# Kernel tuning notes

Hardware: AMD Instinct MI355X
Metric: run time of the kernel (lower is better)

## Reference

```python
import jax, jax.numpy as jnp
import numpy as np

H1, W1GRID, K_SIZE, B = 28, 28, 5, 512
K2 = K_SIZE * K_SIZE  # 25 kernel weight matrices
_BITS = np.array([[0, 0], [0, 1], [1, 0], [1, 1]])  # 2^dim basis combos


def _grid_edges(h, w):
    """8-neighborhood grid graph; returns (src, dst, pseudo in [0,1]^2)."""
    ys, xs = np.meshgrid(np.arange(h), np.arange(w), indexing='ij')
    node = (ys * w + xs).reshape(-1)
    ys, xs = ys.reshape(-1), xs.reshape(-1)
    srcs, dsts, pses = [], [], []
    for dy in (-1, 0, 1):
        for dx in (-1, 0, 1):
            if dy == 0 and dx == 0:
                continue
            ny, nx = ys + dy, xs + dx
            ok = (ny >= 0) & (ny < h) & (nx >= 0) & (nx < w)
            srcs.append((ny * w + nx)[ok])   # neighbor j
            dsts.append(node[ok])            # center i
            p = np.array([[(dx + 1) / 2.0, (dy + 1) / 2.0]], dtype=np.float32)
            pses.append(np.repeat(p, ok.sum(), axis=0))
    return (np.concatenate(srcs), np.concatenate(dsts), np.concatenate(pses))


def _batched_graph(h, w, batch):
    s, d, p = _grid_edges(h, w)
    n = h * w
    off = (np.arange(batch, dtype=np.int64) * n)[:, None]
    src = (s[None, :] + off).reshape(-1)
    dst = (d[None, :] + off).reshape(-1)
    pse = np.tile(p, (batch, 1))
    return np.stack([src, dst]), pse


def setup_inputs() -> dict:
    key = jax.random.key(0)
    ks = jax.random.split(key, 8)
    e1, p1 = _batched_graph(28, 28, B)
    e2, p2 = _batched_graph(14, 14, B)
    return {
        'x': jax.random.uniform(ks[0], (B * 784, 1), jnp.float32),
        'pseudo1': jnp.asarray(p1), 'pseudo2': jnp.asarray(p2),
        'W1': jax.random.normal(ks[1], (K2, 1, 32), jnp.float32) * 0.2,
        'root1': jax.random.normal(ks[2], (1, 32), jnp.float32) * 0.2,
        'b1': jnp.zeros((32,), jnp.float32),
        'W2': jax.random.normal(ks[3], (K2, 32, 64), jnp.float32) * 0.05,
        'root2': jax.random.normal(ks[4], (32, 64), jnp.float32) * 0.05,
        'b2': jnp.zeros((64,), jnp.float32),
        'fc1_w': jax.random.normal(ks[5], (3136, 512), jnp.float32) * 0.02,
        'fc1_b': jnp.zeros((512,), jnp.float32),
        'fc2_w': jax.random.normal(ks[6], (512, 10), jnp.float32) * 0.05,
        'fc2_b': jnp.zeros((10,), jnp.float32),
        'edge_index1': jnp.asarray(e1, jnp.int64 if jax.config.jax_enable_x64 else jnp.int32),
        'edge_index2': jnp.asarray(e2, jnp.int64 if jax.config.jax_enable_x64 else jnp.int32),
    }


def _spline_basis(pseudo, k):
    # open B-spline, degree 1: each dim contributes 2 knots with linear weights
    frac = pseudo * (k - 1)                                   # [E,2]
    lo = jnp.clip(jnp.floor(frac), 0, k - 2)
    f = frac - lo                                             # [E,2]
    w = jnp.stack([1.0 - f, f], axis=-1)                      # [E,2,2]
    idx = jnp.stack([lo, lo + 1], axis=-1).astype(jnp.int32)  # [E,2,2]
    basis = w[:, 0, _BITS[:, 0]] * w[:, 1, _BITS[:, 1]]       # [E,4]
    widx = idx[:, 0, _BITS[:, 0]] + idx[:, 1, _BITS[:, 1]] * k  # [E,4]
    return basis, widx


def _spline_conv(x, edge_index, pseudo, W, root, bias, n_nodes, k):
    src, dst = edge_index[0], edge_index[1]
    x_j = x[src]                                              # [E,Cin] gather
    basis, widx = _spline_basis(pseudo, k)                    # [E,4]
    kk = k * k
    flat = (dst[:, None] * kk + widx).reshape(-1)             # [E*4]
    contrib = (basis[:, :, None] * x_j[:, None, :]).reshape(-1, x.shape[1])
    S = jnp.zeros((n_nodes * kk, x.shape[1]), x.dtype).at[flat].add(contrib)
    S = S.reshape(n_nodes, kk, x.shape[1])                    # per-node per-kernel sums
    deg = jnp.zeros((n_nodes,), x.dtype).at[dst].add(1.0)
    out = jnp.einsum('nki,kio->no', S, W) / jnp.maximum(deg, 1.0)[:, None]
    return out + x @ root + bias


def _pool2x2(x, b, hw, c):
    return x.reshape(b, hw // 2, 2, hw // 2, 2, c).max(axis=(2, 4))


def reference(x, pseudo1, pseudo2, W1, root1, b1, W2, root2, b2,
              fc1_w, fc1_b, fc2_w, fc2_b, edge_index1, edge_index2):
    n1 = x.shape[0]
    b = n1 // 784
    h = jax.nn.elu(_spline_conv(x, edge_index1, pseudo1, W1, root1, b1, n1, K_SIZE))
    h = _pool2x2(h, b, 28, 32).reshape(-1, 32)                # [B*196,32]
    h = jax.nn.elu(_spline_conv(h, edge_index2, pseudo2, W2, root2, b2, b * 196, K_SIZE))
    h = _pool2x2(h, b, 14, 64).reshape(-1, 7 * 7 * 64)        # [B,3136]
    h = jax.nn.elu(h @ fc1_w + fc1_b)
    # dropout is identity in eval mode
    h = jax.nn.elu(h @ fc2_w + fc2_b)
    return jax.nn.log_softmax(h, axis=-1)
```

## Files before the change

### kernel.cpp

```cpp
#include <hip/hip_runtime.h>
#include <math.h>

#define BATCH 512

__device__ __forceinline__ float elu1(float v) {
    return v > 0.f ? v : expm1f(v);
}

__global__ __launch_bounds__(256) void k1_conv1_pool(
    const float* __restrict__ x, const float* __restrict__ W1,
    const float* __restrict__ root1, const float* __restrict__ b1,
    float* __restrict__ p1) {
    __shared__ float xs[900];
    __shared__ float w1s[8 * 32 + 64];
    const int b = blockIdx.x;
    const int t = threadIdx.x;

    for (int l = t; l < 900; l += 256) xs[l] = 0.f;
    {
        int d = t >> 5, c = t & 31;
        int e = d + (d >= 4 ? 1 : 0);
        int dy = e / 3 - 1, dx = e % 3 - 1;
        int widx = 2 * (dx + 1) + 10 * (dy + 1);
        w1s[t] = W1[widx * 32 + c];
        if (t < 32) { w1s[256 + t] = root1[t]; w1s[288 + t] = b1[t]; }
    }
    __syncthreads();
    const float* xb = x + (size_t)b * 784;
    for (int l = t; l < 784; l += 256) {
        int y = l / 28, xx = l % 28;
        xs[(y + 1) * 30 + xx + 1] = xb[l];
    }
    __syncthreads();

    if (t >= 196) return;
    int py = t / 14, px = t % 14;
    int xbse[4];
    float xc[4], inv[4];
    #pragma unroll
    for (int p = 0; p < 4; ++p) {
        int sy = p >> 1, sx = p & 1;
        int y = 2 * py + sy, xx = 2 * px + sx;
        xbse[p] = (y + 1) * 30 + xx + 1;
        xc[p] = xs[xbse[p]];
        int nvy = 3 - (y == 0) - (y == 27);
        int nvx = 3 - (xx == 0) - (xx == 27);
        inv[p] = 1.f / (float)(nvy * nvx - 1);
    }
    const float4* w4 = (const float4*)w1s;
    float* outp = p1 + ((size_t)b * 196 + t) * 32;

    #pragma unroll
    for (int h = 0; h < 2; ++h) {
        float4 acc[4][4];
        #pragma unroll
        for (int p = 0; p < 4; ++p)
            #pragma unroll
            for (int q = 0; q < 4; ++q) acc[p][q] = make_float4(0.f, 0.f, 0.f, 0.f);
        #pragma unroll
        for (int d = 0; d < 8; ++d) {
            int e = d + (d >= 4 ? 1 : 0);
            int od = (e / 3 - 1) * 30 + (e % 3 - 1);
            float4 w0 = w4[d * 8 + h * 4 + 0];
            float4 w1 = w4[d * 8 + h * 4 + 1];
            float4 w2 = w4[d * 8 + h * 4 + 2];
            float4 w3 = w4[d * 8 + h * 4 + 3];
            #pragma unroll
            for (int p = 0; p < 4; ++p) {
                float xv = xs[xbse[p] + od];
                acc[p][0].x += xv * w0.x; acc[p][0].y += xv * w0.y; acc[p][0].z += xv * w0.z; acc[p][0].w += xv * w0.w;
                acc[p][1].x += xv * w1.x; acc[p][1].y += xv * w1.y; acc[p][1].z += xv * w1.z; acc[p][1].w += xv * w1.w;
                acc[p][2].x += xv * w2.x; acc[p][2].y += xv * w2.y; acc[p][2].z += xv * w2.z; acc[p][2].w += xv * w2.w;
                acc[p][3].x += xv * w3.x; acc[p][3].y += xv * w3.y; acc[p][3].z += xv * w3.z; acc[p][3].w += xv * w3.w;
            }
        }
        #pragma unroll
        for (int q = 0; q < 4; ++q) {
            float4 rt = w4[64 + h * 4 + q];
            float4 bs = w4[72 + h * 4 + q];
            float4 m = make_float4(-1e30f, -1e30f, -1e30f, -1e30f);
            #pragma unroll
            for (int p = 0; p < 4; ++p) {
                float4 v;
                v.x = elu1(acc[p][q].x * inv[p] + xc[p] * rt.x + bs.x);
                v.y = elu1(acc[p][q].y * inv[p] + xc[p] * rt.y + bs.y);
                v.z = elu1(acc[p][q].z * inv[p] + xc[p] * rt.z + bs.z);
                v.w = elu1(acc[p][q].w * inv[p] + xc[p] * rt.w + bs.w);
                m.x = fmaxf(m.x, v.x); m.y = fmaxf(m.y, v.y);
                m.z = fmaxf(m.z, v.z); m.w = fmaxf(m.w, v.w);
            }
            *(float4*)(outp + h * 16 + q * 4) = m;
        }
    }
}

__global__ __launch_bounds__(256) void k2_conv2_pool(
    const float* __restrict__ p1, const float* __restrict__ W2,
    const float* __restrict__ root2, const float* __restrict__ b2,
    float* __restrict__ p2) {
    __shared__ float xs[9216];
    __shared__ float wb[2][2176];
    const int b = blockIdx.x;
    const int t = threadIdx.x;
    const int cell = t >> 2, cg = t & 3;
    const int coff = cg * 16 + (cg >> 1) * 4;

    {
        const float4* s4 = (const float4*)W2;
        float4* w4p = (float4*)wb[0];
        #pragma unroll
        for (int j = 0; j < 2; ++j) {
            int l = t + j * 256;
            int i = l >> 4, c4 = l & 15, g = c4 >> 2, q = c4 & 3;
            w4p[i * 17 + g * 4 + (g >> 1) + q] = s4[l];
        }
    }
    for (int l = t; l < 9216; l += 256) xs[l] = 0.f;
    __syncthreads();
    {
        const float* src = p1 + (size_t)b * 6272;
        for (int l = t; l < 6272; l += 256) {
            int node = l >> 5, i = l & 31;
            int y = node / 14, xx = node - y * 14;
            int np = (y + 1) * 16 + xx + 1;
            xs[np * 36 + 4 * ((i >> 2) ^ ((np >> 4) & 7)) + (i & 3)] = src[l];
        }
    }
    __syncthreads();

    const int ccell = (cell < 49) ? cell : 48;
    const int py = ccell / 7, px = ccell - py * 7;
    int npv[4];
    float inv[4];
    #pragma unroll
    for (int p = 0; p < 4; ++p) {
        int sy = p >> 1, sx = p & 1;
        int y = 2 * py + sy, xx = 2 * px + sx;
        npv[p] = (y + 1) * 16 + xx + 1;
        int nvy = 3 - (y == 0) - (y == 13);
        int nvx = 3 - (xx == 0) - (xx == 13);
        inv[p] = 1.f / (float)(nvy * nvx - 1);
    }

    float4 acc[4][4];
    #pragma unroll
    for (int p = 0; p < 4; ++p)
        #pragma unroll
        for (int q = 0; q < 4; ++q) acc[p][q] = make_float4(0.f, 0.f, 0.f, 0.f);

    for (int d = 0; d < 9; ++d) {
        float4 pf0, pf1;
        if (d < 8) {
            int nd = d + 1;
            const float* nsrc;
            if (nd == 8) nsrc = root2;
            else {
                int e = nd + (nd >= 4 ? 1 : 0);
                int dy = e / 3 - 1, dx = e % 3 - 1;
                nsrc = W2 + (size_t)(2 * (dx + 1) + 10 * (dy + 1)) * 2048;
            }
            pf0 = ((const float4*)nsrc)[t];
            pf1 = ((const float4*)nsrc)[t + 256];
        }
        if (d == 8) {
            #pragma unroll
            for (int p = 0; p < 4; ++p) {
                acc[p][0].x *= inv[p]; acc[p][0].y *= inv[p]; acc[p][0].z *= inv[p]; acc[p][0].w *= inv[p];
                acc[p][1].x *= inv[p]; acc[p][1].y *= inv[p]; acc[p][1].z *= inv[p]; acc[p][1].w *= inv[p];
                acc[p][2].x *= inv[p]; acc[p][2].y *= inv[p]; acc[p][2].z *= inv[p]; acc[p][2].w *= inv[p];
                acc[p][3].x *= inv[p]; acc[p][3].y *= inv[p]; acc[p][3].z *= inv[p]; acc[p][3].w *= inv[p];
            }
        }
        int dnode = 0;
        if (d < 8) {
            int e = d + (d >= 4 ? 1 : 0);
            dnode = (e / 3 - 1) * 16 + (e % 3 - 1);
        }
        int xb0, xb1, xb2, xb3, sz0, sz1, sz2, sz3;
        {
            int n0 = npv[0] + dnode, n1 = npv[1] + dnode,
                n2 = npv[2] + dnode, n3 = npv[3] + dnode;
            xb0 = n0 * 36; sz0 = (n0 >> 4) & 7;
            xb1 = n1 * 36; sz1 = (n1 >> 4) & 7;
            xb2 = n2 * 36; sz2 = (n2 >> 4) & 7;
            xb3 = n3 * 36; sz3 = (n3 >> 4) & 7;
        }
        const float* wcur = wb[d & 1] + coff;
        #pragma unroll 2
        for (int i4 = 0; i4 < 8; ++i4) {
            float4 xv0 = *(const float4*)(xs + xb0 + 4 * (i4 ^ sz0));
            float4 xv1 = *(const float4*)(xs + xb1 + 4 * (i4 ^ sz1));
            float4 xv2 = *(const float4*)(xs + xb2 + 4 * (i4 ^ sz2));
            float4 xv3 = *(const float4*)(xs + xb3 + 4 * (i4 ^ sz3));
            float xa0[4] = {xv0.x, xv0.y, xv0.z, xv0.w};
            float xa1[4] = {xv1.x, xv1.y, xv1.z, xv1.w};
            float xa2[4] = {xv2.x, xv2.y, xv2.z, xv2.w};
            float xa3[4] = {xv3.x, xv3.y, xv3.z, xv3.w};
            #pragma unroll
            for (int ii = 0; ii < 4; ++ii) {
                const float* wrow = wcur + (i4 * 4 + ii) * 68;
                float4 w0 = *(const float4*)(wrow + 0);
                float4 w1 = *(const float4*)(wrow + 4);
                float4 w2 = *(const float4*)(wrow + 8);
                float4 w3 = *(const float4*)(wrow + 12);
                float x0 = xa0[ii], x1 = xa1[ii], x2 = xa2[ii], x3 = xa3[ii];
                acc[0][0].x += x0 * w0.x; acc[0][0].y += x0 * w0.y; acc[0][0].z += x0 * w0.z; acc[0][0].w += x0 * w0.w;
                acc[0][1].x += x0 * w1.x; acc[0][1].y += x0 * w1.y; acc[0][1].z += x0 * w1.z; acc[0][1].w += x0 * w1.w;
                acc[0][2].x += x0 * w2.x; acc[0][2].y += x0 * w2.y; acc[0][2].z += x0 * w2.z; acc[0][2].w += x0 * w2.w;
                acc[0][3].x += x0 * w3.x; acc[0][3].y += x0 * w3.y; acc[0][3].z += x0 * w3.z; acc[0][3].w += x0 * w3.w;
                acc[1][0].x += x1 * w0.x; acc[1][0].y += x1 * w0.y; acc[1][0].z += x1 * w0.z; acc[1][0].w += x1 * w0.w;
                acc[1][1].x += x1 * w1.x; acc[1][1].y += x1 * w1.y; acc[1][1].z += x1 * w1.z; acc[1][1].w += x1 * w1.w;
                acc[1][2].x += x1 * w2.x; acc[1][2].y += x1 * w2.y; acc[1][2].z += x1 * w2.z; acc[1][2].w += x1 * w2.w;
                acc[1][3].x += x1 * w3.x; acc[1][3].y += x1 * w3.y; acc[1][3].z += x1 * w3.z; acc[1][3].w += x1 * w3.w;
                acc[2][0].x += x2 * w0.x; acc[2][0].y += x2 * w0.y; acc[2][0].z += x2 * w0.z; acc[2][0].w += x2 * w0.w;
                acc[2][1].x += x2 * w1.x; acc[2][1].y += x2 * w1.y; acc[2][1].z += x2 * w1.z; acc[2][1].w += x2 * w1.w;
                acc[2][2].x += x2 * w2.x; acc[2][2].y += x2 * w2.y; acc[2][2].z += x2 * w2.z; acc[2][2].w += x2 * w2.w;
                acc[2][3].x += x2 * w3.x; acc[2][3].y += x2 * w3.y; acc[2][3].z += x2 * w3.z; acc[2][3].w += x2 * w3.w;
                acc[3][0].x += x3 * w0.x; acc[3][0].y += x3 * w0.y; acc[3][0].z += x3 * w0.z; acc[3][0].w += x3 * w0.w;
                acc[3][1].x += x3 * w1.x; acc[3][1].y += x3 * w1.y; acc[3][1].z += x3 * w1.z; acc[3][1].w += x3 * w1.w;
                acc[3][2].x += x3 * w2.x; acc[3][2].y += x3 * w2.y; acc[3][2].z += x3 * w2.z; acc[3][2].w += x3 * w2.w;
                acc[3][3].x += x3 * w3.x; acc[3][3].y += x3 * w3.y; acc[3][3].z += x3 * w3.z; acc[3][3].w += x3 * w3.w;
            }
        }
        if (d < 8) {
            float4* wn = (float4*)wb[(d + 1) & 1];
            #pragma unroll
            for (int j = 0; j < 2; ++j) {
                int l = t + j * 256;
                int i = l >> 4, c4 = l & 15, g = c4 >> 2, q = c4 & 3;
                wn[i * 17 + g * 4 + (g >> 1) + q] = (j == 0) ? pf0 : pf1;
            }
        }
        __syncthreads();
    }

    if (cell < 49) {
        float* outp = p2 + (size_t)b * 3136 + cell * 64 + cg * 16;
        #pragma unroll
        for (int q = 0; q < 4; ++q) {
            float4 bs = *(const float4*)(b2 + cg * 16 + q * 4);
            float4 m = make_float4(-1e30f, -1e30f, -1e30f, -1e30f);
            #pragma unroll
            for (int p = 0; p < 4; ++p) {
                float4 v;
                v.x = elu1(acc[p][q].x + bs.x);
                v.y = elu1(acc[p][q].y + bs.y);
                v.z = elu1(acc[p][q].z + bs.z);
                v.w = elu1(acc[p][q].w + bs.w);
                m.x = fmaxf(m.x, v.x); m.y = fmaxf(m.y, v.y);
                m.z = fmaxf(m.z, v.z); m.w = fmaxf(m.w, v.w);
            }
            *(float4*)(outp + q * 4) = m;
        }
    }
}

__global__ __launch_bounds__(256) void k3a_fc1(
    const float* __restrict__ A, const float* __restrict__ B,
    float* __restrict__ part, int kchunk) {
    __shared__ float As[2][16][128];
    __shared__ float Bs[2][16][132];
    const int t = threadIdx.x;
    const int tx = t & 15, ty = t >> 4;
    const int n0 = blockIdx.x * 128, m0 = blockIdx.y * 128;
    const int k0 = blockIdx.z * kchunk;
    const int steps = kchunk >> 4;

    const int sm = t & 127, skh = t >> 7;
    const int sk = t >> 4, snq = t & 15;
    const float* Ap = A + (size_t)(m0 + sm) * 3136 + k0 + skh * 8;
    const float* Bp = B + (size_t)(k0 + sk) * 512 + n0 + snq * 8;

    {
        float4 a0 = *(const float4*)Ap;
        float4 a1 = *(const float4*)(Ap + 4);
        float4 b0 = *(const float4*)Bp;
        float4 b1 = *(const float4*)(Bp + 4);
        As[0][skh * 8 + 0][sm] = a0.x; As[0][skh * 8 + 1][sm] = a0.y;
        As[0][skh * 8 + 2][sm] = a0.z; As[0][skh * 8 + 3][sm] = a0.w;
        As[0][skh * 8 + 4][sm] = a1.x; As[0][skh * 8 + 5][sm] = a1.y;
        As[0][skh * 8 + 6][sm] = a1.z; As[0][skh * 8 + 7][sm] = a1.w;
        *(float4*)&Bs[0][sk][snq * 8] = b0;
        *(float4*)&Bs[0][sk][snq * 8 + 4] = b1;
    }
    __syncthreads();

    float acc[8][8];
    #pragma unroll
    for (int r = 0; r < 8; ++r)
        #pragma unroll
        for (int c = 0; c < 8; ++c) acc[r][c] = 0.f;

    for (int s = 0; s < steps; ++s) {
        float4 a0, a1, b0, b1;
        if (s + 1 < steps) {
            a0 = *(const float4*)(Ap + (s + 1) * 16);
            a1 = *(const float4*)(Ap + (s + 1) * 16 + 4);
            b0 = *(const float4*)(Bp + (size_t)(s + 1) * 16 * 512);
            b1 = *(const float4*)(Bp + (size_t)(s + 1) * 16 * 512 + 4);
        }
        const int cur = s & 1;
        #pragma unroll
        for (int k = 0; k < 16; ++k) {
            float4 av0 = *(const float4*)&As[cur][k][ty * 8];
            float4 av1 = *(const float4*)&As[cur][k][ty * 8 + 4];
            float4 bv0 = *(const float4*)&Bs[cur][k][tx * 4];
            float4 bv1 = *(const float4*)&Bs[cur][k][64 + tx * 4];
            float ar[8] = {av0.x, av0.y, av0.z, av0.w, av1.x, av1.y, av1.z, av1.w};
            #pragma unroll
            for (int r = 0; r < 8; ++r) {
                acc[r][0] += ar[r] * bv0.x; acc[r][1] += ar[r] * bv0.y;
                acc[r][2] += ar[r] * bv0.z; acc[r][3] += ar[r] * bv0.w;
                acc[r][4] += ar[r] * bv1.x; acc[r][5] += ar[r] * bv1.y;
                acc[r][6] += ar[r] * bv1.z; acc[r][7] += ar[r] * bv1.w;
            }
        }
        if (s + 1 < steps) {
            const int nxt = cur ^ 1;
            As[nxt][skh * 8 + 0][sm] = a0.x; As[nxt][skh * 8 + 1][sm] = a0.y;
            As[nxt][skh * 8 + 2][sm] = a0.z; As[nxt][skh * 8 + 3][sm] = a0.w;
            As[nxt][skh * 8 + 4][sm] = a1.x; As[nxt][skh * 8 + 5][sm] = a1.y;
            As[nxt][skh * 8 + 6][sm] = a1.z; As[nxt][skh * 8 + 7][sm] = a1.w;
            *(float4*)&Bs[nxt][sk][snq * 8] = b0;
            *(float4*)&Bs[nxt][sk][snq * 8 + 4] = b1;
        }
        __syncthreads();
    }

    float* pbase = part + ((size_t)blockIdx.z * 512 + m0 + ty * 8) * 512 + n0;
    #pragma unroll
    for (int r = 0; r < 8; ++r) {
        float4 o0 = make_float4(acc[r][0], acc[r][1], acc[r][2], acc[r][3]);
        float4 o1 = make_float4(acc[r][4], acc[r][5], acc[r][6], acc[r][7]);
        *(float4*)(pbase + (size_t)r * 512 + tx * 4) = o0;
        *(float4*)(pbase + (size_t)r * 512 + 64 + tx * 4) = o1;
    }
}

__global__ __launch_bounds__(256) void k34_reduce_fc2_lsm(
    const float* __restrict__ part, const float* __restrict__ fc1b,
    const float* __restrict__ w, const float* __restrict__ fc2b,
    float* __restrict__ out, int KZ) {
    __shared__ float red[4][10];
    const int b = blockIdx.x, t = threadIdx.x;

    float a0 = fc1b[t], a1 = fc1b[t + 256];
    for (int kz = 0; kz < KZ; ++kz) {
        const float* pr = part + ((size_t)kz * 512 + b) * 512;
        a0 += pr[t]; a1 += pr[t + 256];
    }
    a0 = elu1(a0); a1 = elu1(a1);

    float acc[10];
    #pragma unroll
    for (int o = 0; o < 10; ++o)
        acc[o] = a0 * w[t * 10 + o] + a1 * w[(t + 256) * 10 + o];
    #pragma unroll
    for (int s = 32; s; s >>= 1)
        #pragma unroll
        for (int o = 0; o < 10; ++o) acc[o] += __shfl_xor(acc[o], s, 64);
    if ((t & 63) == 0) {
        #pragma unroll
        for (int o = 0; o < 10; ++o) red[t >> 6][o] = acc[o];
    }
    __syncthreads();
    if (t == 0) {
        float v[10], m = -1e30f;
        #pragma unroll
        for (int o = 0; o < 10; ++o) {
            float s = red[0][o] + red[1][o] + red[2][o] + red[3][o] + fc2b[o];
            v[o] = elu1(s);
            m = fmaxf(m, v[o]);
        }
        float ssum = 0.f;
        #pragma unroll
        for (int o = 0; o < 10; ++o) ssum += expf(v[o] - m);
        float lse = m + logf(ssum);
        #pragma unroll
        for (int o = 0; o < 10; ++o) out[(size_t)b * 10 + o] = v[o] - lse;
    }
}

extern "C" void kernel_launch(void* const* d_in, const int* in_sizes, int n_in,
                              void* d_out, int out_size, void* d_ws, size_t ws_size,
                              hipStream_t stream) {
    const float* x     = (const float*)d_in[0];
    const float* W1    = (const float*)d_in[3];
    const float* root1 = (const float*)d_in[4];
    const float* b1v   = (const float*)d_in[5];
    const float* W2    = (const float*)d_in[6];
    const float* root2 = (const float*)d_in[7];
    const float* b2v   = (const float*)d_in[8];
    const float* fc1w  = (const float*)d_in[9];
    const float* fc1b  = (const float*)d_in[10];
    const float* fc2w  = (const float*)d_in[11];
    const float* fc2b  = (const float*)d_in[12];

    float* ws = (float*)d_ws;
    float* p1 = ws;
    float* p2 = p1 + (size_t)BATCH * 196 * 32;
    float* tail = p2 + (size_t)BATCH * 49 * 64;

    const size_t base_f = 3211264u + 1605632u;
    int KZ; float* part;
    if (ws_size >= (base_f + 28u * 262144u) * 4u)      { KZ = 28; part = tail; }
    else if (ws_size >= (base_f + 14u * 262144u) * 4u) { KZ = 14; part = tail; }
    else                                               { KZ = 7;  part = p1; }
    const int kchunk = 3136 / KZ;

    k1_conv1_pool<<<dim3(BATCH), 256, 0, stream>>>(x, W1, root1, b1v, p1);
    k2_conv2_pool<<<dim3(BATCH), 256, 0, stream>>>(p1, W2, root2, b2v, p2);
    k3a_fc1<<<dim3(4, 4, KZ), 256, 0, stream>>>(p2, fc1w, part, kchunk);
    k34_reduce_fc2_lsm<<<dim3(BATCH), 256, 0, stream>>>(part, fc1b, fc2w, fc2b, (float*)d_out, KZ);
}
```

Before: 133.7 us.

## Split conv2 output channels across two blocks and shrink fc1 tiles

The conv2 kernel now launches two blocks per image, each computing 32 of the 64 output channels. This halves per-thread accumulators and the weight staging buffer so more blocks run at once. The fc1 split-K GEMM moves from 128x128 tiles with up to 28 K-splits to 64x64 tiles with 12 fixed K-splits of 272, using a 4x4 register tile per thread. This adds parallelism and cuts the partial-sum traffic, but each block reuses less data and conv2 loads its input tile twice.

```diff
diff --git a/kernel.cpp b/kernel.cpp
--- a/kernel.cpp
+++ b/kernel.cpp
@@ -99,21 +99,19 @@
     const float* __restrict__ root2, const float* __restrict__ b2,
     float* __restrict__ p2) {
     __shared__ float xs[9216];
-    __shared__ float wb[2][2176];
-    const int b = blockIdx.x;
+    __shared__ float wb[2][1152];
+    const int b = blockIdx.x >> 1, h = blockIdx.x & 1;
     const int t = threadIdx.x;
     const int cell = t >> 2, cg = t & 3;
-    const int coff = cg * 16 + (cg >> 1) * 4;
-
+    const int coff = cg * 8;
+
+    static const int widx_t[8] = {0, 2, 4, 10, 14, 20, 22, 24};
+
+    const int wi = t >> 3, wc8 = t & 7;
+    const size_t wsrc = (size_t)wi * 64 + h * 32 + wc8 * 4;
     {
-        const float4* s4 = (const float4*)W2;
-        float4* w4p = (float4*)wb[0];
-        #pragma unroll
-        for (int j = 0; j < 2; ++j) {
-            int l = t + j * 256;
-            int i = l >> 4, c4 = l & 15, g = c4 >> 2, q = c4 & 3;
-            w4p[i * 17 + g * 4 + (g >> 1) + q] = s4[l];
-        }
+        float4 v = *(const float4*)(W2 + wsrc);
+        *(float4*)(wb[0] + wi * 36 + wc8 * 4) = v;
     }
     for (int l = t; l < 9216; l += 256) xs[l] = 0.f;
     __syncthreads();
@@ -142,33 +140,22 @@
         inv[p] = 1.f / (float)(nvy * nvx - 1);
     }
 
-    float4 acc[4][4];
-    #pragma unroll
-    for (int p = 0; p < 4; ++p)
-        #pragma unroll
-        for (int q = 0; q < 4; ++q) acc[p][q] = make_float4(0.f, 0.f, 0.f, 0.f);
+    float4 acc[4][2];
+    #pragma unroll
+    for (int p = 0; p < 4; ++p) { acc[p][0] = make_float4(0,0,0,0); acc[p][1] = make_float4(0,0,0,0); }
 
     for (int d = 0; d < 9; ++d) {
-        float4 pf0, pf1;
+        float4 pf;
         if (d < 8) {
             int nd = d + 1;
-            const float* nsrc;
-            if (nd == 8) nsrc = root2;
-            else {
-                int e = nd + (nd >= 4 ? 1 : 0);
-                int dy = e / 3 - 1, dx = e % 3 - 1;
-                nsrc = W2 + (size_t)(2 * (dx + 1) + 10 * (dy + 1)) * 2048;
-            }
-            pf0 = ((const float4*)nsrc)[t];
-            pf1 = ((const float4*)nsrc)[t + 256];
+            const float* nsrc = (nd == 8) ? root2 : (W2 + (size_t)widx_t[nd] * 2048);
+            pf = *(const float4*)(nsrc + wsrc);
         }
         if (d == 8) {
             #pragma unroll
             for (int p = 0; p < 4; ++p) {
                 acc[p][0].x *= inv[p]; acc[p][0].y *= inv[p]; acc[p][0].z *= inv[p]; acc[p][0].w *= inv[p];
                 acc[p][1].x *= inv[p]; acc[p][1].y *= inv[p]; acc[p][1].z *= inv[p]; acc[p][1].w *= inv[p];
-                acc[p][2].x *= inv[p]; acc[p][2].y *= inv[p]; acc[p][2].z *= inv[p]; acc[p][2].w *= inv[p];
-                acc[p][3].x *= inv[p]; acc[p][3].y *= inv[p]; acc[p][3].z *= inv[p]; acc[p][3].w *= inv[p];
             }
         }
         int dnode = 0;
@@ -198,47 +185,31 @@
             float xa3[4] = {xv3.x, xv3.y, xv3.z, xv3.w};
             #pragma unroll
             for (int ii = 0; ii < 4; ++ii) {
-                const float* wrow = wcur + (i4 * 4 + ii) * 68;
+                const float* wrow = wcur + (i4 * 4 + ii) * 36;
                 float4 w0 = *(const float4*)(wrow + 0);
                 float4 w1 = *(const float4*)(wrow + 4);
-                float4 w2 = *(const float4*)(wrow + 8);
-                float4 w3 = *(const float4*)(wrow + 12);
                 float x0 = xa0[ii], x1 = xa1[ii], x2 = xa2[ii], x3 = xa3[ii];
                 acc[0][0].x += x0 * w0.x; acc[0][0].y += x0 * w0.y; acc[0][0].z += x0 * w0.z; acc[0][0].w += x0 * w0.w;
                 acc[0][1].x += x0 * w1.x; acc[0][1].y += x0 * w1.y; acc[0][1].z += x0 * w1.z; acc[0][1].w += x0 * w1.w;
-                acc[0][2].x += x0 * w2.x; acc[0][2].y += x0 * w2.y; acc[0][2].z += x0 * w2.z; acc[0][2].w += x0 * w2.w;
-                acc[0][3].x += x0 * w3.x; acc[0][3].y += x0 * w3.y; acc[0][3].z += x0 * w3.z; acc[0][3].w += x0 * w3.w;
                 acc[1][0].x += x1 * w0.x; acc[1][0].y += x1 * w0.y; acc[1][0].z += x1 * w0.z; acc[1][0].w += x1 * w0.w;
                 acc[1][1].x += x1 * w1.x; acc[1][1].y += x1 * w1.y; acc[1][1].z += x1 * w1.z; acc[1][1].w += x1 * w1.w;
-                acc[1][2].x += x1 * w2.x; acc[1][2].y += x1 * w2.y; acc[1][2].z += x1 * w2.z; acc[1][2].w += x1 * w2.w;
-                acc[1][3].x += x1 * w3.x; acc[1][3].y += x1 * w3.y; acc[1][3].z += x1 * w3.z; acc[1][3].w += x1 * w3.w;
                 acc[2][0].x += x2 * w0.x; acc[2][0].y += x2 * w0.y; acc[2][0].z += x2 * w0.z; acc[2][0].w += x2 * w0.w;
                 acc[2][1].x += x2 * w1.x; acc[2][1].y += x2 * w1.y; acc[2][1].z += x2 * w1.z; acc[2][1].w += x2 * w1.w;
-                acc[2][2].x += x2 * w2.x; acc[2][2].y += x2 * w2.y; acc[2][2].z += x2 * w2.z; acc[2][2].w += x2 * w2.w;
-                acc[2][3].x += x2 * w3.x; acc[2][3].y += x2 * w3.y; acc[2][3].z += x2 * w3.z; acc[2][3].w += x2 * w3.w;
                 acc[3][0].x += x3 * w0.x; acc[3][0].y += x3 * w0.y; acc[3][0].z += x3 * w0.z; acc[3][0].w += x3 * w0.w;
                 acc[3][1].x += x3 * w1.x; acc[3][1].y += x3 * w1.y; acc[3][1].z += x3 * w1.z; acc[3][1].w += x3 * w1.w;
-                acc[3][2].x += x3 * w2.x; acc[3][2].y += x3 * w2.y; acc[3][2].z += x3 * w2.z; acc[3][2].w += x3 * w2.w;
-                acc[3][3].x += x3 * w3.x; acc[3][3].y += x3 * w3.y; acc[3][3].z += x3 * w3.z; acc[3][3].w += x3 * w3.w;
             }
         }
         if (d < 8) {
-            float4* wn = (float4*)wb[(d + 1) & 1];
-            #pragma unroll
-            for (int j = 0; j < 2; ++j) {
-                int l = t + j * 256;
-                int i = l >> 4, c4 = l & 15, g = c4 >> 2, q = c4 & 3;
-                wn[i * 17 + g * 4 + (g >> 1) + q] = (j == 0) ? pf0 : pf1;
-            }
+            *(float4*)(wb[(d + 1) & 1] + wi * 36 + wc8 * 4) = pf;
         }
         __syncthreads();
     }
 
     if (cell < 49) {
-        float* outp = p2 + (size_t)b * 3136 + cell * 64 + cg * 16;
-        #pragma unroll
-        for (int q = 0; q < 4; ++q) {
-            float4 bs = *(const float4*)(b2 + cg * 16 + q * 4);
+        float* outp = p2 + (size_t)b * 3136 + cell * 64 + h * 32 + cg * 8;
+        #pragma unroll
+        for (int q = 0; q < 2; ++q) {
+            float4 bs = *(const float4*)(b2 + h * 32 + cg * 8 + q * 4);
             float4 m = make_float4(-1e30f, -1e30f, -1e30f, -1e30f);
             #pragma unroll
             for (int p = 0; p < 4; ++p) {
@@ -257,84 +228,65 @@
 
 __global__ __launch_bounds__(256) void k3a_fc1(
     const float* __restrict__ A, const float* __restrict__ B,
-    float* __restrict__ part, int kchunk) {
-    __shared__ float As[2][16][128];
-    __shared__ float Bs[2][16][132];
+    float* __restrict__ part) {
+    __shared__ float As[2][16][64];
+    __shared__ float Bs[2][16][72];
     const int t = threadIdx.x;
     const int tx = t & 15, ty = t >> 4;
-    const int n0 = blockIdx.x * 128, m0 = blockIdx.y * 128;
-    const int k0 = blockIdx.z * kchunk;
-    const int steps = kchunk >> 4;
-
-    const int sm = t & 127, skh = t >> 7;
-    const int sk = t >> 4, snq = t & 15;
-    const float* Ap = A + (size_t)(m0 + sm) * 3136 + k0 + skh * 8;
-    const float* Bp = B + (size_t)(k0 + sk) * 512 + n0 + snq * 8;
+    const int n0 = blockIdx.x * 64, m0 = blockIdx.y * 64;
+    const int k0 = blockIdx.z * 272;
+    const int steps = ((blockIdx.z == 11) ? 144 : 272) >> 4;
+
+    const int sm = t & 63, k4 = t >> 6;
+    const int sk = t >> 4, sc = t & 15;
+    const float* Ap = A + (size_t)(m0 + sm) * 3136 + k0 + k4 * 4;
+    const float* Bp = B + (size_t)(k0 + sk) * 512 + n0 + sc * 4;
 
     {
-        float4 a0 = *(const float4*)Ap;
-        float4 a1 = *(const float4*)(Ap + 4);
-        float4 b0 = *(const float4*)Bp;
-        float4 b1 = *(const float4*)(Bp + 4);
-        As[0][skh * 8 + 0][sm] = a0.x; As[0][skh * 8 + 1][sm] = a0.y;
-        As[0][skh * 8 + 2][sm] = a0.z; As[0][skh * 8 + 3][sm] = a0.w;
-        As[0][skh * 8 + 4][sm] = a1.x; As[0][skh * 8 + 5][sm] = a1.y;
-        As[0][skh * 8 + 6][sm] = a1.z; As[0][skh * 8 + 7][sm] = a1.w;
-        *(float4*)&Bs[0][sk][snq * 8] = b0;
-        *(float4*)&Bs[0][sk][snq * 8 + 4] = b1;
-    }
-    __syncthreads();
-
-    float acc[8][8];
-    #pragma unroll
-    for (int r = 0; r < 8; ++r)
-        #pragma unroll
-        for (int c = 0; c < 8; ++c) acc[r][c] = 0.f;
+        float4 av = *(const float4*)Ap;
+        float4 bv = *(const float4*)Bp;
+        As[0][k4 * 4 + 0][sm] = av.x; As[0][k4 * 4 + 1][sm] = av.y;
+        As[0][k4 * 4 + 2][sm] = av.z; As[0][k4 * 4 + 3][sm] = av.w;
+        *(float4*)&Bs[0][sk][sc * 4] = bv;
+    }
+    __syncthreads();
+
+    float acc[4][4];
+    #pragma unroll
+    for (int r = 0; r < 4; ++r)
+        #pragma unroll
+        for (int c = 0; c < 4; ++c) acc[r][c] = 0.f;
 
     for (int s = 0; s < steps; ++s) {
-        float4 a0, a1, b0, b1;
+        float4 a0, b0;
         if (s + 1 < steps) {
             a0 = *(const float4*)(Ap + (s + 1) * 16);
-            a1 = *(const float4*)(Ap + (s + 1) * 16 + 4);
             b0 = *(const float4*)(Bp + (size_t)(s + 1) * 16 * 512);
-            b1 = *(const float4*)(Bp + (size_t)(s + 1) * 16 * 512 + 4);
         }
         const int cur = s & 1;
         #pragma unroll
         for (int k = 0; k < 16; ++k) {
-            float4 av0 = *(const float4*)&As[cur][k][ty * 8];
-            float4 av1 = *(const float4*)&As[cur][k][ty * 8 + 4];
-            float4 bv0 = *(const float4*)&Bs[cur][k][tx * 4];
-            float4 bv1 = *(const float4*)&Bs[cur][k][64 + tx * 4];
-            float ar[8] = {av0.x, av0.y, av0.z, av0.w, av1.x, av1.y, av1.z, av1.w};
-            #pragma unroll
-            for (int r = 0; r < 8; ++r) {
-                acc[r][0] += ar[r] * bv0.x; acc[r][1] += ar[r] * bv0.y;
-                acc[r][2] += ar[r] * bv0.z; acc[r][3] += ar[r] * bv0.w;
-                acc[r][4] += ar[r] * bv1.x; acc[r][5] += ar[r] * bv1.y;
-                acc[r][6] += ar[r] * bv1.z; acc[r][7] += ar[r] * bv1.w;
-            }
+            float4 a4 = *(const float4*)&As[cur][k][ty * 4];
+            float4 b4 = *(const float4*)&Bs[cur][k][tx * 4];
+            acc[0][0] += a4.x * b4.x; acc[0][1] += a4.x * b4.y; acc[0][2] += a4.x * b4.z; acc[0][3] += a4.x * b4.w;
+            acc[1][0] += a4.y * b4.x; acc[1][1] += a4.y * b4.y; acc[1][2] += a4.y * b4.z; acc[1][3] += a4.y * b4.w;
+            acc[2][0] += a4.z * b4.x; acc[2][1] += a4.z * b4.y; acc[2][2] += a4.z * b4.z; acc[2][3] += a4.z * b4.w;
+            acc[3][0] += a4.w * b4.x; acc[3][1] += a4.w * b4.y; acc[3][2] += a4.w * b4.z; acc[3][3] += a4.w * b4.w;
         }
         if (s + 1 < steps) {
             const int nxt = cur ^ 1;
-            As[nxt][skh * 8 + 0][sm] = a0.x; As[nxt][skh * 8 + 1][sm] = a0.y;
-            As[nxt][skh * 8 + 2][sm] = a0.z; As[nxt][skh * 8 + 3][sm] = a0.w;
-            As[nxt][skh * 8 + 4][sm] = a1.x; As[nxt][skh * 8 + 5][sm] = a1.y;
-            As[nxt][skh * 8 + 6][sm] = a1.z; As[nxt][skh * 8 + 7][sm] = a1.w;
-            *(float4*)&Bs[nxt][sk][snq * 8] = b0;
-            *(float4*)&Bs[nxt][sk][snq * 8 + 4] = b1;
+            As[nxt][k4 * 4 + 0][sm] = a0.x; As[nxt][k4 * 4 + 1][sm] = a0.y;
+            As[nxt][k4 * 4 + 2][sm] = a0.z; As[nxt][k4 * 4 + 3][sm] = a0.w;
+            *(float4*)&Bs[nxt][sk][sc * 4] = b0;
         }
         __syncthreads();
     }
 
-    float* pbase = part + ((size_t)blockIdx.z * 512 + m0 + ty * 8) * 512 + n0;
-    #pragma unroll
-    for (int r = 0; r < 8; ++r) {
-        float4 o0 = make_float4(acc[r][0], acc[r][1], acc[r][2], acc[r][3]);
-        float4 o1 = make_float4(acc[r][4], acc[r][5], acc[r][6], acc[r][7]);
-        *(float4*)(pbase + (size_t)r * 512 + tx * 4) = o0;
-        *(float4*)(pbase + (size_t)r * 512 + 64 + tx * 4) = o1;
-    }
+    float* pbase = part + ((size_t)blockIdx.z * 512 + m0 + ty * 4) * 512 + n0;
+    #pragma unroll
+    for (int r = 0; r < 4; ++r)
+        *(float4*)(pbase + (size_t)r * 512 + tx * 4) =
+            make_float4(acc[r][0], acc[r][1], acc[r][2], acc[r][3]);
 }
 
 __global__ __launch_bounds__(256) void k34_reduce_fc2_lsm(
@@ -399,17 +351,10 @@
     float* ws = (float*)d_ws;
     float* p1 = ws;
     float* p2 = p1 + (size_t)BATCH * 196 * 32;
-    float* tail = p2 + (size_t)BATCH * 49 * 64;
-
-    const size_t base_f = 3211264u + 1605632u;
-    int KZ; float* part;
-    if (ws_size >= (base_f + 28u * 262144u) * 4u)      { KZ = 28; part = tail; }
-    else if (ws_size >= (base_f + 14u * 262144u) * 4u) { KZ = 14; part = tail; }
-    else                                               { KZ = 7;  part = p1; }
-    const int kchunk = 3136 / KZ;
+    float* part = p1;
 
     k1_conv1_pool<<<dim3(BATCH), 256, 0, stream>>>(x, W1, root1, b1v, p1);
-    k2_conv2_pool<<<dim3(BATCH), 256, 0, stream>>>(p1, W2, root2, b2v, p2);
-    k3a_fc1<<<dim3(4, 4, KZ), 256, 0, stream>>>(p2, fc1w, part, kchunk);
-    k34_reduce_fc2_lsm<<<dim3(BATCH), 256, 0, stream>>>(part, fc1b, fc2w, fc2b, (float*)d_out, KZ);
-}
+    k2_conv2_pool<<<dim3(2 * BATCH), 256, 0, stream>>>(p1, W2, root2, b2v, p2);
+    k3a_fc1<<<dim3(8, 8, 12), 256, 0, stream>>>(p2, fc1w, part);
+    k34_reduce_fc2_lsm<<<dim3(BATCH), 256, 0, stream>>>(part, fc1b, fc2w, fc2b, (float*)d_out, 12);
+}
```

Result: faster. 128.9 us (-3.6%).
